# Kernel tuning notes

Hardware: AMD Instinct MI355X
Metric: run time of the kernel (lower is better)

The kernel has to match this reference:

```python
import jax, jax.numpy as jnp
import numpy as np

B = 8_388_608  # batch of samples, each a 6-vector -> 3x3 SPD matrix
MIN_VALUE = 1e-12
# lower-triangle scatter indices (orthotropic_indices in the torch module)
INDS_A = jnp.array([0, 1, 1, 2, 2, 2])
INDS_B = jnp.array([0, 0, 1, 0, 1, 2])
IS_DIAG = jnp.array([True, False, True, False, False, True])  # inds_a == inds_b


def setup_inputs() -> dict:
    key = jax.random.key(0)
    x = jax.random.normal(key, (B, 6), dtype=jnp.float32)
    return {"x": x}


def reference(x):
    # positive transform (Softplus) + min_value on diagonal entries only
    x = jnp.where(IS_DIAG, jax.nn.softplus(x) + MIN_VALUE, x)
    # torch.clamp(x[:, [3, 4]], 0, 0) == 0: zero out entries 3 and 4
    x = x.at[:, 3:5].set(0.0)
    # scatter into lower-triangular L: (B, 3, 3)
    L = jnp.zeros((x.shape[0], 3, 3), dtype=x.dtype).at[:, INDS_A, INDS_B].set(x)
    # SPD output L @ L^T
    return jnp.einsum('bij,bkj->bik', L, L)
```

## Files before the change

kernel.cpp:

```cpp
#include <hip/hip_runtime.h>


__device__ __forceinline__ float softplus_f(float x) {
    return fmaxf(x, 0.0f) + __logf(1.0f + __expf(-fabsf(x)));
}

__global__ __launch_bounds__(256) void spd_kernel(const float* __restrict__ x,
                                                  float* __restrict__ out) {
    __shared__ float lin[6 * 256];
    __shared__ float lout[9 * 256];
    const int tid = threadIdx.x;
    const size_t base_in  = (size_t)blockIdx.x * (6 * 256);
    const size_t base_out = (size_t)blockIdx.x * (9 * 256);

#pragma unroll
    for (int k = 0; k < 6; ++k)
        lin[k * 256 + tid] = x[base_in + k * 256 + tid];
    __syncthreads();

    const float x0 = lin[6 * tid + 0];
    const float x1 = lin[6 * tid + 1];
    const float x2 = lin[6 * tid + 2];
    const float x5 = lin[6 * tid + 5];

    const float a = softplus_f(x0) + 1e-12f;
    const float b = x1;
    const float c = softplus_f(x2) + 1e-12f;
    const float f = softplus_f(x5) + 1e-12f;
    const float ab = a * b;

    lout[9 * tid + 0] = a * a;
    lout[9 * tid + 1] = ab;
    lout[9 * tid + 2] = 0.0f;
    lout[9 * tid + 3] = ab;
    lout[9 * tid + 4] = b * b + c * c;
    lout[9 * tid + 5] = 0.0f;
    lout[9 * tid + 6] = 0.0f;
    lout[9 * tid + 7] = 0.0f;
    lout[9 * tid + 8] = f * f;
    __syncthreads();

#pragma unroll
    for (int k = 0; k < 9; ++k)
        out[base_out + k * 256 + tid] = lout[k * 256 + tid];
}

extern "C" void kernel_launch(void* const* d_in, const int* in_sizes, int n_in,
                              void* d_out, int out_size, void* d_ws, size_t ws_size,
                              hipStream_t stream) {
    const float* x = (const float*)d_in[0];
    float* out = (float*)d_out;

    const int B = in_sizes[0] / 6;
    const int block = 256;
    const int grid = B / block;

    spd_kernel<<<grid, block, 0, stream>>>(x, out);
}
```

Before: 94.14 us.

## Vectorize global I/O with float4 nontemporal accesses and two samples per thread

Each block now handles 512 samples with 256 threads. Global loads and stores use 128-bit nontemporal vector accesses, staged through one reused LDS buffer. This cuts the number of memory instructions and block launches and avoids polluting the cache on a streaming workload. The cost is an extra barrier and possible LDS bank conflicts on the strided per-sample accesses.

```diff
diff --git a/kernel.cpp b/kernel.cpp
--- a/kernel.cpp
+++ b/kernel.cpp
@@ -1,48 +1,75 @@
 #include <hip/hip_runtime.h>
 
+
+#define SAMP 512
+#define NTHR 256
+
+typedef float float4n __attribute__((ext_vector_type(4)));
 
 __device__ __forceinline__ float softplus_f(float x) {
     return fmaxf(x, 0.0f) + __logf(1.0f + __expf(-fabsf(x)));
 }
 
-__global__ __launch_bounds__(256) void spd_kernel(const float* __restrict__ x,
-                                                  float* __restrict__ out) {
-    __shared__ float lin[6 * 256];
-    __shared__ float lout[9 * 256];
+__global__ __launch_bounds__(NTHR) void spd_kernel(const float* __restrict__ x,
+                                                   float* __restrict__ out) {
+    __shared__ float lds[9 * SAMP];
+    float4n* lds4 = reinterpret_cast<float4n*>(lds);
     const int tid = threadIdx.x;
-    const size_t base_in  = (size_t)blockIdx.x * (6 * 256);
-    const size_t base_out = (size_t)blockIdx.x * (9 * 256);
 
+    const float4n* in4  = reinterpret_cast<const float4n*>(x) + (size_t)blockIdx.x * (6 * SAMP / 4);
+    float4n*       out4 = reinterpret_cast<float4n*>(out)     + (size_t)blockIdx.x * (9 * SAMP / 4);
+
+    float4n v[3];
 #pragma unroll
-    for (int k = 0; k < 6; ++k)
-        lin[k * 256 + tid] = x[base_in + k * 256 + tid];
+    for (int k = 0; k < 3; ++k)
+        v[k] = __builtin_nontemporal_load(&in4[k * NTHR + tid]);
+#pragma unroll
+    for (int k = 0; k < 3; ++k)
+        lds4[k * NTHR + tid] = v[k];
     __syncthreads();
 
-    const float x0 = lin[6 * tid + 0];
-    const float x1 = lin[6 * tid + 1];
-    const float x2 = lin[6 * tid + 2];
-    const float x5 = lin[6 * tid + 5];
-
-    const float a = softplus_f(x0) + 1e-12f;
-    const float b = x1;
-    const float c = softplus_f(x2) + 1e-12f;
-    const float f = softplus_f(x5) + 1e-12f;
-    const float ab = a * b;
-
-    lout[9 * tid + 0] = a * a;
-    lout[9 * tid + 1] = ab;
-    lout[9 * tid + 2] = 0.0f;
-    lout[9 * tid + 3] = ab;
-    lout[9 * tid + 4] = b * b + c * c;
-    lout[9 * tid + 5] = 0.0f;
-    lout[9 * tid + 6] = 0.0f;
-    lout[9 * tid + 7] = 0.0f;
-    lout[9 * tid + 8] = f * f;
+    float r0[2], r1[2], r2[2], r3[2];
+#pragma unroll
+    for (int j = 0; j < 2; ++j) {
+        const int s = j * NTHR + tid;
+        const float x0 = lds[6 * s + 0];
+        const float x1 = lds[6 * s + 1];
+        const float x2 = lds[6 * s + 2];
+        const float x5 = lds[6 * s + 5];
+        const float a = softplus_f(x0) + 1e-12f;
+        const float c = softplus_f(x2) + 1e-12f;
+        const float f = softplus_f(x5) + 1e-12f;
+        r0[j] = a * a;
+        r1[j] = a * x1;
+        r2[j] = x1 * x1 + c * c;
+        r3[j] = f * f;
+    }
     __syncthreads();
 
 #pragma unroll
-    for (int k = 0; k < 9; ++k)
-        out[base_out + k * 256 + tid] = lout[k * 256 + tid];
+    for (int j = 0; j < 2; ++j) {
+        const int s = j * NTHR + tid;
+        lds[9 * s + 0] = r0[j];
+        lds[9 * s + 1] = r1[j];
+        lds[9 * s + 2] = 0.0f;
+        lds[9 * s + 3] = r1[j];
+        lds[9 * s + 4] = r2[j];
+        lds[9 * s + 5] = 0.0f;
+        lds[9 * s + 6] = 0.0f;
+        lds[9 * s + 7] = 0.0f;
+        lds[9 * s + 8] = r3[j];
+    }
+    __syncthreads();
+
+#pragma unroll
+    for (int k = 0; k < 4; ++k) {
+        float4n w = lds4[k * NTHR + tid];
+        __builtin_nontemporal_store(w, &out4[k * NTHR + tid]);
+    }
+    if (tid < NTHR / 2) {
+        float4n w = lds4[4 * NTHR + tid];
+        __builtin_nontemporal_store(w, &out4[4 * NTHR + tid]);
+    }
 }
 
 extern "C" void kernel_launch(void* const* d_in, const int* in_sizes, int n_in,
@@ -52,8 +79,7 @@
     float* out = (float*)d_out;
 
     const int B = in_sizes[0] / 6;
-    const int block = 256;
-    const int grid = B / block;
+    const int grid = B / SAMP;
 
-    spd_kernel<<<grid, block, 0, stream>>>(x, out);
+    spd_kernel<<<grid, NTHR, 0, stream>>>(x, out);
 }
```

After: 89.36 us. 1.05x faster.
